# Kernel tuning notes

Hardware: AMD Instinct MI355X
Metric: run time of the kernel (lower is better)

Reference implementation:

```python
import jax, jax.numpy as jnp
import numpy as np

HEADS = 8
EPS_LN = 1e-5
EPS_N = 1e-12


def _dw(x, w, b, pad):
    # depthwise conv, NCHW, weight [C,1,kh,kw]
    C = x.shape[1]
    y = jax.lax.conv_general_dilated(x, w, (1, 1), pad,
                                     dimension_numbers=('NCHW', 'OIHW', 'NCHW'),
                                     feature_group_count=C)
    return y + b[None, :, None, None]


def _pw(x, w, b):
    # 1x1 conv as einsum, weight [Cout, Cin]
    return jnp.einsum('bihw,oi->bohw', x, w) + b[None, :, None, None]


def _l2n(x):
    n = jnp.sqrt(jnp.sum(x * x, axis=-1, keepdims=True))
    return x / jnp.maximum(n, EPS_N)


def _axis_attn(q, k, v):
    # q,k,v: [B, heads, N, D]; L2-normalized QK, softmax, +q residual
    q = _l2n(q)
    k = _l2n(k)
    attn = jax.nn.softmax(jnp.einsum('bhnd,bhmd->bhnm', q, k), axis=-1)
    return jnp.einsum('bhnm,bhmd->bhnd', attn, v) + q


def setup_inputs() -> dict:
    key = jax.random.key(0)
    B, C, H, W = 16, 256, 80, 80
    ks = jax.random.split(key, 16)

    def nrm(k, shape, s=0.02):
        return jax.random.normal(k, shape, dtype=jnp.float32) * s

    z = lambda *s: jnp.zeros(s, jnp.float32)
    return {
        'x': nrm(ks[0], (B, C, H, W), 1.0),
        'ln_g': jnp.ones((C,), jnp.float32),
        'ln_b': z(C),
        'w_in': nrm(ks[1], (C, C)), 'b_in': z(C),
        'w_out': nrm(ks[2], (C, C)), 'b_out': z(C),
        'wx7': nrm(ks[3], (C, 1, 1, 7)), 'bx7': z(C),
        'wx11': nrm(ks[4], (C, 1, 1, 11)), 'bx11': z(C),
        'wx21': nrm(ks[5], (C, 1, 1, 21)), 'bx21': z(C),
        'wy7': nrm(ks[6], (C, 1, 7, 1)), 'by7': z(C),
        'wy11': nrm(ks[7], (C, 1, 11, 1)), 'by11': z(C),
        'wy21': nrm(ks[8], (C, 1, 21, 1)), 'by21': z(C),
    }


def reference(x, ln_g, ln_b, w_in, b_in, w_out, b_out,
              wx7, bx7, wx11, bx11, wx21, bx21,
              wy7, by7, wy11, by11, wy21, by21):
    B, C, H, W = x.shape
    cp = C // HEADS

    # LayerNorm over channel dim (applied per-pixel)
    mu = jnp.mean(x, axis=1, keepdims=True)
    var = jnp.var(x, axis=1, keepdims=True)
    xn = (x - mu) / jnp.sqrt(var + EPS_LN)
    xn = xn * ln_g[None, :, None, None] + ln_b[None, :, None, None]

    fx = _pw(_dw(xn, wx7, bx7, ((0, 0), (3, 3)))
             + _dw(xn, wx11, bx11, ((0, 0), (5, 5)))
             + _dw(xn, wx21, bx21, ((0, 0), (10, 10))), w_in, b_in)
    fy = _pw(_dw(xn, wy7, by7, ((3, 3), (0, 0)))
             + _dw(xn, wy11, by11, ((5, 5), (0, 0)))
             + _dw(xn, wy21, by21, ((10, 10), (0, 0))), w_in, b_in)

    def to_h(t):  # [B,C,H,W] -> [B,heads,H,W*cp] (w outer, c inner)
        return t.reshape(B, HEADS, cp, H, W).transpose(0, 1, 3, 4, 2).reshape(B, HEADS, H, W * cp)

    def from_h(t):
        return t.reshape(B, HEADS, H, W, cp).transpose(0, 1, 4, 2, 3).reshape(B, C, H, W)

    def to_w(t):  # [B,C,H,W] -> [B,heads,W,H*cp] (h outer, c inner)
        return t.reshape(B, HEADS, cp, H, W).transpose(0, 1, 4, 3, 2).reshape(B, HEADS, W, H * cp)

    def from_w(t):
        return t.reshape(B, HEADS, W, H, cp).transpose(0, 1, 4, 3, 2).reshape(B, C, H, W)

    out_x = from_h(_axis_attn(to_h(fy), to_h(fx), to_h(fx)))
    out_y = from_w(_axis_attn(to_w(fx), to_w(fy), to_w(fy)))

    return _pw(out_x, w_out, b_out) + _pw(out_y, w_out, b_out) + x
```

## Files before the change

kernel.cpp:

```cpp
#include <hip/hip_runtime.h>

typedef unsigned short u16;
typedef unsigned int   u32;

#define NB  16
#define NC  256
#define NH  80
#define NW  80
#define NHW 6400

typedef short bf16x8 __attribute__((ext_vector_type(8)));
typedef float f32x4  __attribute__((ext_vector_type(4)));

__device__ __forceinline__ float b2f(u16 u) {
  union { u32 i; float f; } c; c.i = ((u32)u) << 16; return c.f;
}
__device__ __forceinline__ u16 f2b(float f) {
  union { float f; u32 i; } c; c.f = f;
  return (u16)((c.i + 0x7FFFu + ((c.i >> 16) & 1u)) >> 16);
}
__device__ __forceinline__ float ldx(const void* p, size_t i, int f32f) {
  return f32f ? ((const float*)p)[i] : b2f(((const u16*)p)[i]);
}
__device__ __forceinline__ int getf(int fh, const int* flagp) {
  return (fh >= 0) ? fh : *flagp;
}

__global__ void probe_init(int* __restrict__ flag) { flag[0] = 0; flag[1] = 0; }

__global__ __launch_bounds__(256) void probe_count(const u16* __restrict__ x,
                                                   int* __restrict__ flag)
{
  __shared__ int cnt[256];
  int base = (blockIdx.x * 256 + threadIdx.x) * 16;
  int c = 0;
  uint4 v0 = *(const uint4*)(x + base);
  uint4 v1 = *(const uint4*)(x + base + 8);
  u32 w[8] = {v0.x, v0.y, v0.z, v0.w, v1.x, v1.y, v1.z, v1.w};
  #pragma unroll
  for (int j = 0; j < 8; j++) {
    if (((w[j] >> 7)  & 0xFFu) == 0xFFu) c++;
    if (((w[j] >> 23) & 0xFFu) == 0xFFu) c++;
  }
  cnt[threadIdx.x] = c; __syncthreads();
  for (int s = 128; s > 0; s >>= 1) {
    if (threadIdx.x < s) cnt[threadIdx.x] += cnt[threadIdx.x + s];
    __syncthreads();
  }
  if (threadIdx.x == 0) atomicAdd(&flag[1], cnt[0]);
}

__global__ void probe_decide(int* __restrict__ flag) {
  flag[0] = (flag[1] > 16) ? 1 : 0;
}

struct CvtArgs { const void* src[18]; int cum[19]; };

__global__ __launch_bounds__(256) void cvt_weights(CvtArgs a, float* __restrict__ dst,
                                                   int fh, const int* __restrict__ flagp)
{
  int f = getf(fh, flagp);
  int i = blockIdx.x * 256 + threadIdx.x;
  int s = 0;
  while (i >= a.cum[s + 1]) s++;
  int j = i - a.cum[s];
  float v = f ? ((const float*)a.src[s])[j] : b2f(((const u16*)a.src[s])[j]);
  if (!(v == v) || fabsf(v) > 1e30f) v = 0.f;
  dst[i] = v;
}

__global__ __launch_bounds__(256) void split_w(const float* __restrict__ w_in,
    const float* __restrict__ w_out, u16* __restrict__ WB)
{
  int i = blockIdx.x * 256 + threadIdx.x;
  int mat = i >> 16, idx = i & 65535;
  float v = (mat ? w_out : w_in)[idx];
  u16 hi = f2b(v);
  u16 lo = f2b(v - b2f(hi));
  WB[mat * 131072 + idx] = hi;
  WB[mat * 131072 + 65536 + idx] = lo;
}

__global__ __launch_bounds__(256) void ln_stats(const void* __restrict__ xsrc,
    size_t xoff, int fh, const int* __restrict__ flagp, float2* __restrict__ stats)
{
  int f = getf(fh, flagp);
  int bl = blockIdx.y;
  int p4 = blockIdx.x * 1024 + threadIdx.x * 4;
  if (p4 >= NHW) return;
  size_t base = xoff + (size_t)bl * NC * NHW + p4;
  float s1[4] = {0.f, 0.f, 0.f, 0.f}, s2[4] = {0.f, 0.f, 0.f, 0.f};
  if (f) {
    const float* xp = (const float*)xsrc + base;
    for (int c = 0; c < NC; c++) {
      float4 v = *(const float4*)(xp + (size_t)c * NHW);
      s1[0] += v.x; s2[0] += v.x * v.x;
      s1[1] += v.y; s2[1] += v.y * v.y;
      s1[2] += v.z; s2[2] += v.z * v.z;
      s1[3] += v.w; s2[3] += v.w * v.w;
    }
  } else {
    const u16* xp = (const u16*)xsrc + base;
    for (int c = 0; c < NC; c++) {
      ushort4 v = *(const ushort4*)(xp + (size_t)c * NHW);
      float a = b2f(v.x), b = b2f(v.y), cc = b2f(v.z), d = b2f(v.w);
      s1[0] += a;  s2[0] += a * a;
      s1[1] += b;  s2[1] += b * b;
      s1[2] += cc; s2[2] += cc * cc;
      s1[3] += d;  s2[3] += d * d;
    }
  }
  float2* so = stats + (size_t)bl * NHW + p4;
  #pragma unroll
  for (int j = 0; j < 4; j++) {
    float mean = s1[j] * (1.f / 256.f);
    float var  = s2[j] * (1.f / 256.f) - mean * mean;
    so[j] = make_float2(mean, rsqrtf(var + 1e-5f));
  }
}

__global__ __launch_bounds__(256) void dw_both(const void* __restrict__ xsrc,
    size_t xoff, int fh, const int* __restrict__ flagp,
    const float2* __restrict__ stats,
    const float* __restrict__ g, const float* __restrict__ bt,
    const float* __restrict__ wx7,  const float* __restrict__ bx7,
    const float* __restrict__ wx11, const float* __restrict__ bx11,
    const float* __restrict__ wx21, const float* __restrict__ bx21,
    const float* __restrict__ wy7,  const float* __restrict__ by7,
    const float* __restrict__ wy11, const float* __restrict__ by11,
    const float* __restrict__ wy21, const float* __restrict__ by21,
    u16* __restrict__ sx, u16* __restrict__ sy)
{
  __shared__ float xnp[80][116];
  __shared__ float cwx[21], cwy[21];
  __shared__ float cbs[2];
  int f = getf(fh, flagp);
  int bc = blockIdx.x;
  int c  = bc & 255;
  int bl = bc >> 8;
  int t = threadIdx.x;
  if (t < 21) {
    float v = wx21[c * 21 + t];
    if (t >= 5 && t <= 15) v += wx11[c * 11 + t - 5];
    if (t >= 7 && t <= 13) v += wx7[c * 7 + t - 7];
    cwx[t] = v;
  } else if (t < 42) {
    int j = t - 21;
    float v = wy21[c * 21 + j];
    if (j >= 5 && j <= 15) v += wy11[c * 11 + j - 5];
    if (j >= 7 && j <= 13) v += wy7[c * 7 + j - 7];
    cwy[j] = v;
  } else if (t == 42) { cbs[0] = bx7[c] + bx11[c] + bx21[c]; }
  else if (t == 43)   { cbs[1] = by7[c] + by11[c] + by21[c]; }
  for (int i = t; i < 2560; i += 256) {
    int rr = i >> 5, cc = i & 31;
    xnp[rr][cc < 16 ? cc : 80 + cc] = 0.f;
  }
  float cg = g[c], cbt = bt[c];
  size_t xrow = xoff + (size_t)bc * NHW;
  const float2* st = stats + (size_t)bl * NHW;
  for (int i = t; i < NHW; i += 256) {
    float v = ldx(xsrc, xrow + i, f);
    float2 s = st[i];
    xnp[i / 80][16 + i % 80] = (v - s.x) * s.y * cg + cbt;
  }
  __syncthreads();
  float bxv = cbs[0], byv = cbs[1];
  size_t obase = (size_t)bc * NHW;
  for (int u = t; u < 800; u += 256) {
    int h = u / 10, w0 = (u % 10) * 8;
    float r[32];
    #pragma unroll
    for (int j = 0; j < 8; j++)
      *(float4*)&r[4 * j] = *(const float4*)&xnp[h][w0 + 4 + 4 * j];
    float ax[8], ay[8];
    #pragma unroll
    for (int j = 0; j < 8; j++) { ax[j] = bxv; ay[j] = byv; }
    #pragma unroll
    for (int dd = 0; dd < 21; dd++) {
      float wv = cwx[dd];
      #pragma unroll
      for (int j = 0; j < 8; j++) ax[j] += wv * r[j + 2 + dd];
    }
    #pragma unroll
    for (int dd = 0; dd < 21; dd++) {
      int hp = h + dd - 10;
      int hc = min(max(hp, 0), 79);
      float wv = (hp == hc) ? cwy[dd] : 0.f;
      float4 v0 = *(const float4*)&xnp[hc][16 + w0];
      float4 v1 = *(const float4*)&xnp[hc][20 + w0];
      ay[0] += wv * v0.x; ay[1] += wv * v0.y; ay[2] += wv * v0.z; ay[3] += wv * v0.w;
      ay[4] += wv * v1.x; ay[5] += wv * v1.y; ay[6] += wv * v1.z; ay[7] += wv * v1.w;
    }
    size_t ob = obase + h * 80 + w0;
    ushort4 a0, a1, b0, b1;
    a0.x = f2b(ax[0]); a0.y = f2b(ax[1]); a0.z = f2b(ax[2]); a0.w = f2b(ax[3]);
    a1.x = f2b(ax[4]); a1.y = f2b(ax[5]); a1.z = f2b(ax[6]); a1.w = f2b(ax[7]);
    b0.x = f2b(ay[0]); b0.y = f2b(ay[1]); b0.z = f2b(ay[2]); b0.w = f2b(ay[3]);
    b1.x = f2b(ay[4]); b1.y = f2b(ay[5]); b1.z = f2b(ay[6]); b1.w = f2b(ay[7]);
    *(ushort4*)(sx + ob)     = a0;
    *(ushort4*)(sx + ob + 4) = a1;
    *(ushort4*)(sy + ob)     = b0;
    *(ushort4*)(sy + ob + 4) = b1;
  }
}

template<int FINAL>
__global__ __launch_bounds__(256) void pw_mfma_t(const u16* __restrict__ WB,
    u16* io0, u16* io1, const float* __restrict__ bias,
    void* __restrict__ OutBase, size_t out_off,
    const void* __restrict__ xsrc, size_t xoff,
    int fh, const int* __restrict__ flagp)
{
  __shared__ u16 S[16384];
  u16* InT = S;
  int bl = blockIdx.y;
  int p0 = blockIdx.x * 64;
  int t  = threadIdx.x;
  int lane = t & 63, wid = t >> 6, lg = lane >> 4, lr = lane & 15;
  u16* io = (FINAL || blockIdx.z == 0) ? io0 : io1;

  {
    int kb = t >> 3, pb = t & 7;
    const u16* src = io + (size_t)bl * NC * NHW + p0 + pb * 8;
    u32 r[8][4];
    #pragma unroll
    for (int i = 0; i < 8; i++) {
      uint4 v = *(const uint4*)(src + (size_t)(kb * 8 + i) * NHW);
      r[i][0] = v.x; r[i][1] = v.y; r[i][2] = v.z; r[i][3] = v.w;
    }
    #pragma unroll
    for (int j = 0; j < 8; j++) {
      u32 w[4];
      #pragma unroll
      for (int m = 0; m < 4; m++) {
        u32 a = r[2 * m][j >> 1], b = r[2 * m + 1][j >> 1];
        w[m] = (j & 1) ? ((a >> 16) | (b & 0xFFFF0000u))
                       : ((a & 0xFFFFu) | (b << 16));
      }
      int p = pb * 8 + j;
      *(uint4*)&InT[p * 256 + ((kb ^ ((j ^ pb) & 7)) * 8)] = make_uint4(w[0], w[1], w[2], w[3]);
    }
  }
  __syncthreads();

  f32x4 acc[4][4];
  #pragma unroll
  for (int m = 0; m < 4; m++)
    #pragma unroll
    for (int n = 0; n < 4; n++)
      acc[m][n] = (f32x4){0.f, 0.f, 0.f, 0.f};

  const u16* wa = WB + ((wid * 4) * 16 + lr) * 256 + lg * 8;
  #pragma unroll 2
  for (int ch = 0; ch < 8; ch++) {
    bf16x8 bfr[4];
    #pragma unroll
    for (int n = 0; n < 4; n++) {
      int px = n * 16 + lr;
      int fpx = (px ^ (px >> 3)) & 7;
      bfr[n] = *(const bf16x8*)&InT[px * 256 + (((ch * 4 + lg) ^ fpx) * 8)];
    }
    #pragma unroll
    for (int m = 0; m < 4; m++) {
      const u16* wrow = wa + m * 16 * 256 + ch * 32;
      bf16x8 ahi = *(const bf16x8*)(wrow);
      bf16x8 alo = *(const bf16x8*)(wrow + 65536);
      #pragma unroll
      for (int n = 0; n < 4; n++) {
        acc[m][n] = __builtin_amdgcn_mfma_f32_16x16x32_bf16(ahi, bfr[n], acc[m][n], 0, 0, 0);
        acc[m][n] = __builtin_amdgcn_mfma_f32_16x16x32_bf16(alo, bfr[n], acc[m][n], 0, 0, 0);
      }
    }
  }
  __syncthreads();

  if (FINAL) {
    float* Otf = (float*)S;
    int f = getf(fh, flagp);
    #pragma unroll
    for (int h = 0; h < 2; h++) {
      if ((wid >> 1) == h) {
        #pragma unroll
        for (int m = 0; m < 4; m++)
          #pragma unroll
          for (int r = 0; r < 4; r++) {
            int o  = (wid * 4 + m) * 16 + 4 * lg + r;
            int ol = o & 127;
            float bv = 2.f * bias[o];
            #pragma unroll
            for (int n = 0; n < 4; n++) {
              int px = n * 16 + lr;
              Otf[ol * 64 + (px ^ ((ol & 7) * 8))] = acc[m][n][r] + bv;
            }
          }
      }
      __syncthreads();
      int rl = t >> 1, seg = (t & 1) * 32;
      int o = h * 128 + rl;
      size_t gbase = ((size_t)bl * NC + o) * NHW + p0 + seg;
      #pragma unroll
      for (int j2 = 0; j2 < 8; j2++) {
        int cj = (seg + 4 * j2) ^ ((rl & 7) * 8);
        float4 v = *(float4*)&Otf[rl * 64 + cj];
        size_t gi = gbase + j2 * 4;
        if (f) {
          const float* xp = (const float*)xsrc + xoff + gi;
          v.x += xp[0]; v.y += xp[1]; v.z += xp[2]; v.w += xp[3];
          *(float4*)((float*)OutBase + out_off + gi) = v;
        } else {
          ushort4 xv = *(const ushort4*)((const u16*)xsrc + xoff + gi);
          ushort4 ov;
          ov.x = f2b(v.x + b2f(xv.x)); ov.y = f2b(v.y + b2f(xv.y));
          ov.z = f2b(v.z + b2f(xv.z)); ov.w = f2b(v.w + b2f(xv.w));
          *(ushort4*)((u16*)OutBase + out_off + gi) = ov;
        }
      }
      __syncthreads();
    }
  } else {
    u16* Ot = S;
    #pragma unroll
    for (int m = 0; m < 4; m++)
      #pragma unroll
      for (int r = 0; r < 4; r++) {
        int o = (wid * 4 + m) * 16 + 4 * lg + r;
        float bv = bias[o];
        #pragma unroll
        for (int n = 0; n < 4; n++) {
          int px = n * 16 + lr;
          Ot[o * 64 + (px ^ ((o & 7) * 8))] = f2b(acc[m][n][r] + bv);
        }
      }
    __syncthreads();
    u16* orow = io + ((size_t)bl * NC + t) * NHW + p0;
    #pragma unroll
    for (int j = 0; j < 8; j++) {
      uint4 v = *(uint4*)&Ot[t * 64 + ((j ^ (t & 7)) * 8)];
      *(uint4*)(orow + j * 8) = v;
    }
  }
  (void)OutBase; (void)out_off; (void)xsrc; (void)xoff; (void)flagp; (void)io1;
}

__global__ __launch_bounds__(256) void transpose_sumsq(const u16* __restrict__ fx,
    const u16* __restrict__ fy, u16* __restrict__ fxT, u16* __restrict__ fyT,
    float* __restrict__ rs_fx, float* __restrict__ rs_fy,
    float* __restrict__ cs_fx, float* __restrict__ cs_fy)
{
  __shared__ u16 tile[80][81];
  int pl = blockIdx.x, ten = blockIdx.y;
  const u16* src = (ten ? fy : fx) + (size_t)pl * NHW;
  u16*       dst = (ten ? fyT : fxT) + (size_t)pl * NHW;
  int t = threadIdx.x;
  for (int i = t; i < NHW; i += 256) tile[i / 80][i % 80] = src[i];
  __syncthreads();
  for (int i = t; i < NHW; i += 256) dst[i] = tile[i % 80][i / 80];
  if (t < 80) {
    float s = 0.f;
    #pragma unroll
    for (int k = 0; k < 80; k++) { float v = b2f(tile[t][k]); s += v * v; }
    (ten ? rs_fy : rs_fx)[pl * 80 + t] = s;
  } else if (t < 160) {
    int w = t - 80; float s = 0.f;
    #pragma unroll
    for (int h = 0; h < 80; h++) { float v = b2f(tile[h][w]); s += v * v; }
    (ten ? cs_fy : cs_fx)[pl * 80 + w] = s;
  }
}

__global__ __launch_bounds__(256) void norm_combine(const float* __restrict__ rs_fx,
    const float* __restrict__ rs_fy, const float* __restrict__ cs_fx,
    const float* __restrict__ cs_fy, float* __restrict__ invn, int Nb)
{
  int t = blockIdx.x * 256 + threadIdx.x;
  int blk = Nb * 640;
  int side = t / blk, r = t % blk;
  int b = r / 640, rem = r % 640, hd = rem / 80, row = rem % 80;
  const float* src = (side == 0) ? rs_fy : (side == 1) ? rs_fx : (side == 2) ? cs_fx : cs_fy;
  size_t base = (size_t)(b * 256 + hd * 32) * 80 + row;
  float s = 0.f;
  #pragma unroll
  for (int ci = 0; ci < 32; ci++) s += src[base + ci * 80];
  invn[t] = 1.f / fmaxf(sqrtf(s), 1e-12f);
}

template<int T0, int NT>
__device__ __forceinline__ void gram_wave(const u16* pa, const u16* pb,
                                          int lg, int lr, f32x4* acc)
{
  constexpr int MLO = T0 / 5;
  #pragma unroll
  for (int ch = 0; ch < 3; ch++) {
    bool tz = (ch == 2) && (lg >= 2);
    int kk = ch * 32 + 8 * lg;
    if (tz) kk = 0;
    bf16x8 af[2], bf[5];
    #pragma unroll
    for (int m = 0; m < 2; m++)
      af[m] = *(const bf16x8*)(pa + ((MLO + m) * 16 + lr) * 80 + kk);
    #pragma unroll
    for (int n = 0; n < 5; n++)
      bf[n] = *(const bf16x8*)(pb + (n * 16 + lr) * 80 + kk);
    if (tz) {
      bf16x8 z = {0, 0, 0, 0, 0, 0, 0, 0};
      af[0] = z; af[1] = z;
    }
    #pragma unroll
    for (int j = 0; j < NT; j++) {
      acc[j] = __builtin_amdgcn_mfma_f32_16x16x32_bf16(
          af[(T0 + j) / 5 - MLO], bf[(T0 + j) % 5], acc[j], 0, 0, 0);
    }
  }
}

template<int T0, int NT>
__device__ __forceinline__ void gram_all(const u16* Ab, const u16* Bb,
                                         int lg, int lr, f32x4* acc)
{
  for (int ci = 0; ci < 32; ci++)
    gram_wave<T0, NT>(Ab + (size_t)ci * NHW, Bb + (size_t)ci * NHW, lg, lr, acc);
}

__global__ __launch_bounds__(256) void gram_softmax_mfma(const u16* __restrict__ fx,
    const u16* __restrict__ fy, const u16* __restrict__ fxT, const u16* __restrict__ fyT,
    const float* __restrict__ invn, u16* __restrict__ Sbuf, int Nb)
{
  __shared__ float At[80][81];
  int hd = blockIdx.x, b = blockIdx.y, axis = blockIdx.z;
  size_t sl0 = (size_t)(b * 256 + hd * 32) * NHW;
  const u16* Ab = (axis ? fxT : fy) + sl0;
  const u16* Bb = (axis ? fyT : fx) + sl0;
  int t = threadIdx.x, lane = t & 63, wid = t >> 6;
  int lg = lane >> 4, lr = lane & 15;
  f32x4 acc0 = {0.f, 0.f, 0.f, 0.f};
  f32x4 acc[7];
  #pragma unroll
  for (int j = 0; j < 7; j++) acc[j] = acc0;
  if      (wid == 0) gram_all<0, 7>(Ab, Bb, lg, lr, acc);
  else if (wid == 1) gram_all<7, 6>(Ab, Bb, lg, lr, acc);
  else if (wid == 2) gram_all<13, 6>(Ab, Bb, lg, lr, acc);
  else               gram_all<19, 6>(Ab, Bb, lg, lr, acc);
  int blk = Nb * 640;
  int rowbase = (b * 8 + hd) * 80;
  const float* invq = invn + (axis ? 2 * blk : 0)   + rowbase;
  const float* invk = invn + (axis ? 3 * blk : blk) + rowbase;
  int t0  = wid ? 6 * wid + 1 : 0;
  int cnt = wid ? 6 : 7;
  #pragma unroll
  for (int j = 0; j < 7; j++) {
    if (j < cnt) {
      int tt = t0 + j, m = tt / 5, n = tt % 5;
      int col = n * 16 + lr;
      float ik = invk[col];
      #pragma unroll
      for (int r = 0; r < 4; r++) {
        int row = m * 16 + 4 * lg + r;
        float gv = acc[j][r] * invq[row] * ik;
        At[row][col] = fminf(fmaxf(gv, -8.f), 8.f);
      }
    }
  }
  __syncthreads();
  u16* Sg = Sbuf + ((size_t)(axis * Nb * 8 + b * 8 + hd)) * NHW;
  if (t < 80) {
    float mx = -1e30f;
    for (int j = 0; j < 80; j++) mx = fmaxf(mx, At[t][j]);
    float s = 0.f;
    for (int j = 0; j < 80; j++) s += __expf(At[t][j] - mx);
    float inv = 1.f / s;
    for (int j = 0; j < 80; j++) Sg[t * 80 + j] = f2b(__expf(At[t][j] - mx) * inv);
  }
}

template<int T0, int NT>
__device__ __forceinline__ void apply_wave(const u16* SH, const u16* fxT,
    const u16* fyP, const u16* SW, int lg, int lr, f32x4* acc)
{
  constexpr int MLO = T0 / 5;
  for (int ch = 0; ch < 3; ch++) {
    bool tz = (ch == 2) && (lg >= 2);
    int kk = ch * 32 + 8 * lg;
    if (tz) kk = 0;
    bf16x8 a1[2], a2[2], b1[5], b2[5];
    #pragma unroll
    for (int m = 0; m < 2; m++) {
      a1[m] = *(const bf16x8*)(SH  + ((MLO + m) * 16 + lr) * 80 + kk);
      a2[m] = *(const bf16x8*)(fyP + ((MLO + m) * 16 + lr) * 80 + kk);
    }
    #pragma unroll
    for (int n = 0; n < 5; n++) {
      b1[n] = *(const bf16x8*)(fxT + (n * 16 + lr) * 80 + kk);
      b2[n] = *(const bf16x8*)(SW  + (n * 16 + lr) * 80 + kk);
    }
    if (tz) {
      bf16x8 z = {0, 0, 0, 0, 0, 0, 0, 0};
      a1[0] = z; a1[1] = z; a2[0] = z; a2[1] = z;
    }
    #pragma unroll
    for (int j = 0; j < NT; j++) {
      acc[j] = __builtin_amdgcn_mfma_f32_16x16x32_bf16(
          a1[(T0 + j) / 5 - MLO], b1[(T0 + j) % 5], acc[j], 0, 0, 0);
      acc[j] = __builtin_amdgcn_mfma_f32_16x16x32_bf16(
          a2[(T0 + j) / 5 - MLO], b2[(T0 + j) % 5], acc[j], 0, 0, 0);
    }
  }
}

__global__ __launch_bounds__(256, 2) void apply_hw_mfma(const u16* __restrict__ fy_g,
    const u16* __restrict__ fxT_g, const u16* __restrict__ Sbuf,
    const float* __restrict__ invn, u16* fx_io, int Nb)
{
  int ci = blockIdx.x, hd = blockIdx.y, b = blockIdx.z;
  size_t off = (size_t)(b * 256 + hd * 32 + ci) * NHW;
  const u16* SgH = Sbuf + (size_t)(b * 8 + hd) * NHW;
  const u16* SgW = Sbuf + ((size_t)(Nb * 8) + b * 8 + hd) * NHW;
  const u16* fyP = fy_g + off;
  const u16* fxT = fxT_g + off;
  int t = threadIdx.x, lane = t & 63, wid = t >> 6;
  int lg = lane >> 4, lr = lane & 15;
  f32x4 acc0 = {0.f, 0.f, 0.f, 0.f};
  f32x4 acc[7];
  #pragma unroll
  for (int j = 0; j < 7; j++) acc[j] = acc0;
  if      (wid == 0) apply_wave<0, 7>(SgH, fxT, fyP, SgW, lg, lr, acc);
  else if (wid == 1) apply_wave<7, 6>(SgH, fxT, fyP, SgW, lg, lr, acc);
  else if (wid == 2) apply_wave<13, 6>(SgH, fxT, fyP, SgW, lg, lr, acc);
  else               apply_wave<19, 6>(SgH, fxT, fyP, SgW, lg, lr, acc);
  const float* invqH = invn + (b * 8 + hd) * 80;
  const float* invqW = invn + 2 * Nb * 640 + (b * 8 + hd) * 80;
  int t0  = wid ? 6 * wid + 1 : 0;
  int cnt = wid ? 6 : 7;
  #pragma unroll
  for (int j = 0; j < 7; j++) {
    if (j < cnt) {
      int tt = t0 + j, m = tt / 5, n = tt % 5;
      int col = n * 16 + lr;
      float ivW = invqW[col];
      #pragma unroll
      for (int r = 0; r < 4; r++) {
        int row = m * 16 + 4 * lg + r;
        size_t ix = off + row * 80 + col;
        float v = acc[j][r] + b2f(fy_g[ix]) * invqH[row] + b2f(fx_io[ix]) * ivW;
        fx_io[ix] = f2b(v);
      }
    }
  }
}

extern "C" void kernel_launch(void* const* d_in, const int* in_sizes, int n_in,
                              void* d_out, int out_size, void* d_ws, size_t ws_size,
                              hipStream_t stream) {
  const int wsz[18] = {256, 256, 65536, 256, 65536, 256,
                       1792, 256, 2816, 256, 5376, 256,
                       1792, 256, 2816, 256, 5376, 256};
  CvtArgs ca;
  int cum = 0;
  for (int i = 0; i < 18; i++) { ca.src[i] = d_in[i + 1]; ca.cum[i] = cum; cum += wsz[i]; }
  ca.cum[18] = cum;

  int hostf = -1;
  if (in_sizes && n_in > 0) {
    if      (in_sizes[0] == 104857600) hostf = 1;
    else if (in_sizes[0] == 52428800)  hostf = 0;
  }
  if (hostf < 0) {
    if      (out_size == 104857600) hostf = 1;
    else if (out_size == 52428800)  hostf = 0;
  }

  int Nb = 1;
  for (int cand = 16; cand >= 1; cand >>= 1) {
    size_t need = (size_t)cand * 13701120 + 614416 + 524288;
    if (need <= ws_size) { Nb = cand; break; }
  }
  char* p = (char*)d_ws;
  int*    flag  = (int*)p;    p += 16;
  float*  wbuf  = (float*)p;  p += 614400;
  u16*    wsplit= (u16*)p;    p += 524288;
  u16*    fxbuf = (u16*)p;    p += (size_t)Nb * 3276800;
  u16*    fybuf = (u16*)p;    p += (size_t)Nb * 3276800;
  u16*    fxT   = (u16*)p;    p += (size_t)Nb * 3276800;
  u16*    fyT   = (u16*)p;    p += (size_t)Nb * 3276800;
  float2* stats = (float2*)p; p += (size_t)Nb * 51200;
  float*  rs_fx = (float*)p;  p += (size_t)Nb * 81920;
  float*  rs_fy = (float*)p;  p += (size_t)Nb * 81920;
  float*  cs_fx = (float*)p;  p += (size_t)Nb * 81920;
  float*  cs_fy = (float*)p;  p += (size_t)Nb * 81920;
  float*  invn  = (float*)p;  p += (size_t)Nb * 10240;
  u16*    Sbuf  = (u16*)p;

  float* ln_g = wbuf + ca.cum[0];  float* ln_b = wbuf + ca.cum[1];
  float* w_in = wbuf + ca.cum[2];  float* b_in = wbuf + ca.cum[3];
  float* w_out= wbuf + ca.cum[4]; float* b_out= wbuf + ca.cum[5];
  float* wx7  = wbuf + ca.cum[6];  float* bx7  = wbuf + ca.cum[7];
  float* wx11 = wbuf + ca.cum[8];  float* bx11 = wbuf + ca.cum[9];
  float* wx21 = wbuf + ca.cum[10]; float* bx21 = wbuf + ca.cum[11];
  float* wy7  = wbuf + ca.cum[12]; float* by7  = wbuf + ca.cum[13];
  float* wy11 = wbuf + ca.cum[14]; float* by11 = wbuf + ca.cum[15];
  float* wy21 = wbuf + ca.cum[16]; float* by21 = wbuf + ca.cum[17];

  if (hostf < 0) {
    probe_init<<<dim3(1), dim3(1), 0, stream>>>(flag);
    probe_count<<<dim3(64), dim3(256), 0, stream>>>((const u16*)d_in[0], flag);
    probe_decide<<<dim3(1), dim3(1), 0, stream>>>(flag);
  }
  cvt_weights<<<dim3(600), dim3(256), 0, stream>>>(ca, wbuf, hostf, flag);
  split_w<<<dim3(512), dim3(256), 0, stream>>>(w_in, w_out, wsplit);

  for (int b0 = 0; b0 < NB; b0 += Nb) {
    size_t xoff = (size_t)b0 * NC * NHW;

    ln_stats<<<dim3(7, Nb), dim3(256), 0, stream>>>(d_in[0], xoff, hostf, flag, stats);
    dw_both<<<dim3(Nb * 256), dim3(256), 0, stream>>>(d_in[0], xoff, hostf, flag, stats,
        ln_g, ln_b, wx7, bx7, wx11, bx11, wx21, bx21,
        wy7, by7, wy11, by11, wy21, by21, fxbuf, fybuf);
    pw_mfma_t<0><<<dim3(100, Nb, 2), dim3(256), 0, stream>>>(wsplit, fxbuf, fybuf,
        b_in, nullptr, 0, nullptr, 0, hostf, flag);
    transpose_sumsq<<<dim3(Nb * 256, 2), dim3(256), 0, stream>>>(fxbuf, fybuf, fxT, fyT,
        rs_fx, rs_fy, cs_fx, cs_fy);
    norm_combine<<<dim3(10 * Nb), dim3(256), 0, stream>>>(rs_fx, rs_fy, cs_fx, cs_fy, invn, Nb);
    gram_softmax_mfma<<<dim3(8, Nb, 2), dim3(256), 0, stream>>>(fxbuf, fybuf, fxT, fyT, invn, Sbuf, Nb);
    apply_hw_mfma<<<dim3(32, 8, Nb), dim3(256), 0, stream>>>(fybuf, fxT, Sbuf, invn, fxbuf, Nb);
    pw_mfma_t<1><<<dim3(100, Nb, 1), dim3(256), 0, stream>>>(wsplit + 131072, fxbuf, nullptr,
        b_out, d_out, xoff, d_in[0], xoff, hostf, flag);
  }
  (void)in_sizes; (void)n_in; (void)out_size;
}
```

Measured before the change: 884.2 us.

## Retile pointwise MFMA GEMM to 128-pixel tiles with split-K staging and XCD-aware block mapping

The 1x1-conv MFMA kernel now processes 128-pixel tiles. Input channels are staged through LDS in two K halves of 128. The final projection splits the 256 output channels across two blocks, so each block computes 128 outputs. Launches are flattened to 1D, and block indices are remapped in chunks of eight so neighbouring tiles land on the same XCD for L2 locality. The intent is more weight reuse per load and better cache behaviour, at the cost of more accumulator registers, extra syncs, and a reduced grid size for the first pass.

```diff
diff --git a/kernel.cpp b/kernel.cpp
--- a/kernel.cpp
+++ b/kernel.cpp
@@ -210,66 +210,76 @@
     u16* io0, u16* io1, const float* __restrict__ bias,
     void* __restrict__ OutBase, size_t out_off,
     const void* __restrict__ xsrc, size_t xoff,
-    int fh, const int* __restrict__ flagp)
+    int fh, const int* __restrict__ flagp, int Nb, int chunk)
 {
   __shared__ u16 S[16384];
-  u16* InT = S;
-  int bl = blockIdx.y;
-  int p0 = blockIdx.x * 64;
+  constexpr int MT = FINAL ? 2 : 4;
+  int d = blockIdx.x;
+  int w = chunk ? (d & 7) * chunk + (d >> 3) : d;
+  int oh, px, bl, zz;
+  if (FINAL) {
+    oh = w & 1; int s = w >> 1; px = s % 50; bl = s / 50; zz = 0;
+  } else {
+    oh = 0; px = w % 50; int q = w / 50; bl = q % Nb; zz = q / Nb;
+  }
+  int p0 = px * 128;
   int t  = threadIdx.x;
   int lane = t & 63, wid = t >> 6, lg = lane >> 4, lr = lane & 15;
-  u16* io = (FINAL || blockIdx.z == 0) ? io0 : io1;
-
-  {
-    int kb = t >> 3, pb = t & 7;
-    const u16* src = io + (size_t)bl * NC * NHW + p0 + pb * 8;
-    u32 r[8][4];
-    #pragma unroll
-    for (int i = 0; i < 8; i++) {
-      uint4 v = *(const uint4*)(src + (size_t)(kb * 8 + i) * NHW);
-      r[i][0] = v.x; r[i][1] = v.y; r[i][2] = v.z; r[i][3] = v.w;
-    }
-    #pragma unroll
-    for (int j = 0; j < 8; j++) {
-      u32 w[4];
-      #pragma unroll
-      for (int m = 0; m < 4; m++) {
-        u32 a = r[2 * m][j >> 1], b = r[2 * m + 1][j >> 1];
-        w[m] = (j & 1) ? ((a >> 16) | (b & 0xFFFF0000u))
-                       : ((a & 0xFFFFu) | (b << 16));
-      }
-      int p = pb * 8 + j;
-      *(uint4*)&InT[p * 256 + ((kb ^ ((j ^ pb) & 7)) * 8)] = make_uint4(w[0], w[1], w[2], w[3]);
-    }
-  }
-  __syncthreads();
-
-  f32x4 acc[4][4];
-  #pragma unroll
-  for (int m = 0; m < 4; m++)
-    #pragma unroll
-    for (int n = 0; n < 4; n++)
+  u16* io = (FINAL || zz == 0) ? io0 : io1;
+
+  f32x4 acc[MT][8];
+  #pragma unroll
+  for (int m = 0; m < MT; m++)
+    #pragma unroll
+    for (int n = 0; n < 8; n++)
       acc[m][n] = (f32x4){0.f, 0.f, 0.f, 0.f};
 
-  const u16* wa = WB + ((wid * 4) * 16 + lr) * 256 + lg * 8;
-  #pragma unroll 2
-  for (int ch = 0; ch < 8; ch++) {
-    bf16x8 bfr[4];
-    #pragma unroll
-    for (int n = 0; n < 4; n++) {
-      int px = n * 16 + lr;
-      int fpx = (px ^ (px >> 3)) & 7;
-      bfr[n] = *(const bf16x8*)&InT[px * 256 + (((ch * 4 + lg) ^ fpx) * 8)];
-    }
-    #pragma unroll
-    for (int m = 0; m < 4; m++) {
-      const u16* wrow = wa + m * 16 * 256 + ch * 32;
-      bf16x8 ahi = *(const bf16x8*)(wrow);
-      bf16x8 alo = *(const bf16x8*)(wrow + 65536);
-      #pragma unroll
-      for (int n = 0; n < 4; n++) {
-        acc[m][n] = __builtin_amdgcn_mfma_f32_16x16x32_bf16(ahi, bfr[n], acc[m][n], 0, 0, 0);
-        acc[m][n] = __builtin_amdgcn_mfma_f32_16x16x32_bf16(alo, bfr[n], acc[m][n], 0, 0, 0);
+  for (int kh = 0; kh < 2; kh++) {
+    if (kh) __syncthreads();
+    {
+      int kb = t >> 4, pb = t & 15;
+      const u16* src = io + ((size_t)bl * NC + kh * 128 + kb * 8) * NHW + p0 + pb * 8;
+      u32 r[8][4];
+      #pragma unroll
+      for (int i = 0; i < 8; i++) {
+        uint4 v = *(const uint4*)(src + (size_t)i * NHW);
+        r[i][0] = v.x; r[i][1] = v.y; r[i][2] = v.z; r[i][3] = v.w;
+      }
+      #pragma unroll
+      for (int j = 0; j < 8; j++) {
+        u32 wv[4];
+        #pragma unroll
+        for (int m = 0; m < 4; m++) {
+          u32 a = r[2 * m][j >> 1], b = r[2 * m + 1][j >> 1];
+          wv[m] = (j & 1) ? ((a >> 16) | (b & 0xFFFF0000u))
+                          : ((a & 0xFFFFu) | (b << 16));
+        }
+        int pp = pb * 8 + j;
+        int gg = ((pp >> 3) ^ pp) & 15;
+        *(uint4*)&S[pp * 128 + ((kb ^ gg) & 15) * 8] = make_uint4(wv[0], wv[1], wv[2], wv[3]);
+      }
+    }
+    __syncthreads();
+    #pragma unroll
+    for (int chl = 0; chl < 4; chl++) {
+      int kglob = kh * 128 + chl * 32;
+      #pragma unroll
+      for (int m = 0; m < MT; m++) {
+        int o = (FINAL ? oh * 128 : 0) + (wid * MT + m) * 16 + lr;
+        const u16* wrow = WB + (size_t)o * 256 + kglob + lg * 8;
+        bf16x8 ahi = *(const bf16x8*)(wrow);
+        bf16x8 alo = *(const bf16x8*)(wrow + 65536);
+        #pragma unroll
+        for (int ng = 0; ng < 4; ng++) {
+          int pxa = (ng * 2) * 16 + lr, pxb = pxa + 16;
+          int ka = chl * 4 + lg;
+          bf16x8 b0 = *(const bf16x8*)&S[pxa * 128 + ((ka ^ (((pxa >> 3) ^ pxa) & 15)) & 15) * 8];
+          bf16x8 b1 = *(const bf16x8*)&S[pxb * 128 + ((ka ^ (((pxb >> 3) ^ pxb) & 15)) & 15) * 8];
+          acc[m][ng * 2]     = __builtin_amdgcn_mfma_f32_16x16x32_bf16(ahi, b0, acc[m][ng * 2], 0, 0, 0);
+          acc[m][ng * 2]     = __builtin_amdgcn_mfma_f32_16x16x32_bf16(alo, b0, acc[m][ng * 2], 0, 0, 0);
+          acc[m][ng * 2 + 1] = __builtin_amdgcn_mfma_f32_16x16x32_bf16(ahi, b1, acc[m][ng * 2 + 1], 0, 0, 0);
+          acc[m][ng * 2 + 1] = __builtin_amdgcn_mfma_f32_16x16x32_bf16(alo, b1, acc[m][ng * 2 + 1], 0, 0, 0);
+        }
       }
     }
   }
@@ -282,28 +292,29 @@
     for (int h = 0; h < 2; h++) {
       if ((wid >> 1) == h) {
         #pragma unroll
-        for (int m = 0; m < 4; m++)
+        for (int m = 0; m < 2; m++)
           #pragma unroll
           for (int r = 0; r < 4; r++) {
-            int o  = (wid * 4 + m) * 16 + 4 * lg + r;
-            int ol = o & 127;
-            float bv = 2.f * bias[o];
+            int ol = (wid * 2 + m) * 16 + 4 * lg + r;
+            int ro = ol & 63;
+            float bv = 2.f * bias[oh * 128 + ol];
             #pragma unroll
-            for (int n = 0; n < 4; n++) {
-              int px = n * 16 + lr;
-              Otf[ol * 64 + (px ^ ((ol & 7) * 8))] = acc[m][n][r] + bv;
+            for (int n = 0; n < 8; n++) {
+              int pxn = n * 16 + lr;
+              int cuf = (pxn >> 2) ^ (ro & 7);
+              Otf[ro * 128 + cuf * 4 + (pxn & 3)] = acc[m][n][r] + bv;
             }
           }
       }
       __syncthreads();
-      int rl = t >> 1, seg = (t & 1) * 32;
-      int o = h * 128 + rl;
-      size_t gbase = ((size_t)bl * NC + o) * NHW + p0 + seg;
-      #pragma unroll
-      for (int j2 = 0; j2 < 8; j2++) {
-        int cj = (seg + 4 * j2) ^ ((rl & 7) * 8);
-        float4 v = *(float4*)&Otf[rl * 64 + cj];
-        size_t gi = gbase + j2 * 4;
+      int row = t >> 2, q = t & 3;
+      size_t gbase = ((size_t)bl * NC + oh * 128 + h * 64 + row) * NHW + p0 + q * 32;
+      #pragma unroll
+      for (int j = 0; j < 8; j++) {
+        int uf = q * 8 + j;
+        int cuf = uf ^ (row & 7);
+        float4 v = *(float4*)&Otf[row * 128 + cuf * 4];
+        size_t gi = gbase + j * 4;
         if (f) {
           const float* xp = (const float*)xsrc + xoff + gi;
           v.x += xp[0]; v.y += xp[1]; v.z += xp[2]; v.w += xp[3];
@@ -321,23 +332,32 @@
   } else {
     u16* Ot = S;
     #pragma unroll
-    for (int m = 0; m < 4; m++)
-      #pragma unroll
-      for (int r = 0; r < 4; r++) {
-        int o = (wid * 4 + m) * 16 + 4 * lg + r;
-        float bv = bias[o];
+    for (int h = 0; h < 2; h++) {
+      if ((wid >> 1) == h) {
         #pragma unroll
-        for (int n = 0; n < 4; n++) {
-          int px = n * 16 + lr;
-          Ot[o * 64 + (px ^ ((o & 7) * 8))] = f2b(acc[m][n][r] + bv);
-        }
-      }
-    __syncthreads();
-    u16* orow = io + ((size_t)bl * NC + t) * NHW + p0;
-    #pragma unroll
-    for (int j = 0; j < 8; j++) {
-      uint4 v = *(uint4*)&Ot[t * 64 + ((j ^ (t & 7)) * 8)];
-      *(uint4*)(orow + j * 8) = v;
+        for (int m = 0; m < 4; m++)
+          #pragma unroll
+          for (int r = 0; r < 4; r++) {
+            int o  = (wid * 4 + m) * 16 + 4 * lg + r;
+            int ol = o & 127;
+            float bv = bias[o];
+            #pragma unroll
+            for (int n = 0; n < 8; n++) {
+              int pxn = n * 16 + lr;
+              int cu = ((pxn >> 3) + (ol & 7)) & 15;
+              Ot[ol * 128 + cu * 8 + (pxn & 7)] = f2b(acc[m][n][r] + bv);
+            }
+          }
+      }
+      __syncthreads();
+      int row = t >> 1, half = t & 1;
+      u16* orow = io + ((size_t)bl * NC + h * 128 + row) * NHW + p0 + half * 64;
+      #pragma unroll
+      for (int j = 0; j < 8; j++) {
+        int cu = ((half * 8 + j) + (row & 7)) & 15;
+        *(uint4*)(orow + j * 8) = *(uint4*)&Ot[row * 128 + cu * 8];
+      }
+      __syncthreads();
     }
   }
   (void)OutBase; (void)out_off; (void)xsrc; (void)xoff; (void)flagp; (void)io1;
@@ -608,6 +628,9 @@
   cvt_weights<<<dim3(600), dim3(256), 0, stream>>>(ca, wbuf, hostf, flag);
   split_w<<<dim3(512), dim3(256), 0, stream>>>(w_in, w_out, wsplit);
 
+  int Gpw = 100 * Nb;
+  int chunk = (Gpw % 8 == 0) ? Gpw / 8 : 0;
+
   for (int b0 = 0; b0 < NB; b0 += Nb) {
     size_t xoff = (size_t)b0 * NC * NHW;
 
@@ -615,15 +638,15 @@
     dw_both<<<dim3(Nb * 256), dim3(256), 0, stream>>>(d_in[0], xoff, hostf, flag, stats,
         ln_g, ln_b, wx7, bx7, wx11, bx11, wx21, bx21,
         wy7, by7, wy11, by11, wy21, by21, fxbuf, fybuf);
-    pw_mfma_t<0><<<dim3(100, Nb, 2), dim3(256), 0, stream>>>(wsplit, fxbuf, fybuf,
-        b_in, nullptr, 0, nullptr, 0, hostf, flag);
+    pw_mfma_t<0><<<dim3(Gpw), dim3(256), 0, stream>>>(wsplit, fxbuf, fybuf,
+        b_in, nullptr, 0, nullptr, 0, hostf, flag, Nb, chunk);
     transpose_sumsq<<<dim3(Nb * 256, 2), dim3(256), 0, stream>>>(fxbuf, fybuf, fxT, fyT,
         rs_fx, rs_fy, cs_fx, cs_fy);
     norm_combine<<<dim3(10 * Nb), dim3(256), 0, stream>>>(rs_fx, rs_fy, cs_fx, cs_fy, invn, Nb);
     gram_softmax_mfma<<<dim3(8, Nb, 2), dim3(256), 0, stream>>>(fxbuf, fybuf, fxT, fyT, invn, Sbuf, Nb);
     apply_hw_mfma<<<dim3(32, 8, Nb), dim3(256), 0, stream>>>(fybuf, fxT, Sbuf, invn, fxbuf, Nb);
-    pw_mfma_t<1><<<dim3(100, Nb, 1), dim3(256), 0, stream>>>(wsplit + 131072, fxbuf, nullptr,
-        b_out, d_out, xoff, d_in[0], xoff, hostf, flag);
+    pw_mfma_t<1><<<dim3(Gpw), dim3(256), 0, stream>>>(wsplit + 131072, fxbuf, nullptr,
+        b_out, d_out, xoff, d_in[0], xoff, hostf, flag, Nb, chunk);
   }
   (void)in_sizes; (void)n_in; (void)out_size;
 }
```

Result: faster. 864.4 us (-2.2%).
